# Kernel optimization log

Measured on AMD Instinct MI355X. Metric: run time of the kernel, lower is better.

Reference implementation:

```python
import jax, jax.numpy as jnp
import numpy as np

V, E, H, L = 32000, 256, 512, 2
B, S, T = 32, 128, 128

def _run_lstm(xs, layers, h0, c0):
    # xs: [B,T,in]; layers: list of (Wih[4H,in], Whh[4H,H], bih[4H], bhh[4H]); h0,c0: [L,B,H]
    def step(carry, x):
        h, c = carry
        inp = x
        hs, cs = [], []
        for l, (Wih, Whh, bih, bhh) in enumerate(layers):
            g = inp @ Wih.T + h[l] @ Whh.T + bih + bhh
            i, f, gg, o = jnp.split(g, 4, axis=-1)  # torch gate order: i, f, g, o
            cn = jax.nn.sigmoid(f) * c[l] + jax.nn.sigmoid(i) * jnp.tanh(gg)
            hn = jax.nn.sigmoid(o) * jnp.tanh(cn)
            hs.append(hn); cs.append(cn); inp = hn
        return (jnp.stack(hs), jnp.stack(cs)), inp
    (hT, cT), ys = jax.lax.scan(step, (h0, c0), jnp.swapaxes(xs, 0, 1))
    return jnp.swapaxes(ys, 0, 1), hT, cT

def setup_inputs():
    key = jax.random.key(0)
    ks = jax.random.split(key, 24)
    k = 1.0 / np.sqrt(H)
    u = lambda kk, shape: jax.random.uniform(kk, shape, jnp.float32, -k, k)
    inp = {
        "src": jax.random.randint(ks[0], (B, S), 0, V),
        "tgt": jax.random.randint(ks[1], (B, T), 0, V),
        "emb": jax.random.normal(ks[2], (V, E), jnp.float32) * 0.02,
        "Wout": u(ks[3], (V, H)),
        "bout": u(ks[4], (V,)),
    }
    i = 5
    for pre in ("enc", "dec"):
        for l in range(L):
            din = E if l == 0 else H
            inp[pre + "_Wih" + str(l)] = u(ks[i], (4 * H, din)); i += 1
            inp[pre + "_Whh" + str(l)] = u(ks[i], (4 * H, H)); i += 1
            inp[pre + "_bih" + str(l)] = u(ks[i], (4 * H,)); i += 1
            inp[pre + "_bhh" + str(l)] = u(ks[i], (4 * H,)); i += 1
    return inp

def reference(src, tgt, emb, Wout, bout,
              enc_Wih0, enc_Whh0, enc_bih0, enc_bhh0,
              enc_Wih1, enc_Whh1, enc_bih1, enc_bhh1,
              dec_Wih0, dec_Whh0, dec_bih0, dec_bhh0,
              dec_Wih1, dec_Whh1, dec_bih1, dec_bhh1):
    enc_layers = [(enc_Wih0, enc_Whh0, enc_bih0, enc_bhh0),
                  (enc_Wih1, enc_Whh1, enc_bih1, enc_bhh1)]
    dec_layers = [(dec_Wih0, dec_Whh0, dec_bih0, dec_bhh0),
                  (dec_Wih1, dec_Whh1, dec_bih1, dec_bhh1)]
    h0 = jnp.zeros((L, src.shape[0], H), jnp.float32)
    c0 = jnp.zeros_like(h0)
    src_embed = emb[src]                                   # [B,S,E]; dropout = identity (eval)
    _, hT, cT = _run_lstm(src_embed, enc_layers, h0, c0)
    tgt_embed = emb[tgt]                                   # full teacher forcing (ratio=1.0)
    dec_out, _, _ = _run_lstm(tgt_embed, dec_layers, hT, cT)  # [B,T,H]
    logits = jnp.einsum('bth,vh->btv', dec_out, Wout) + bout  # [B,T,V]
    return logits
```

## Files before the change

kernel.cpp:

```cpp
#include <hip/hip_runtime.h>
#include <math.h>

#define Bsz 32
#define Hd  512
#define SEQ 128
#define G4H 2048
#define BARSTRIDE 32
#define SLOT 16384

typedef __attribute__((ext_vector_type(8))) short bf16x8;
typedef __attribute__((ext_vector_type(4))) float f32x4;
typedef __attribute__((ext_vector_type(4))) unsigned short us4;

__device__ __forceinline__ void gload16(const void* g, void* l) {
  __builtin_amdgcn_global_load_lds(
      (const __attribute__((address_space(1))) unsigned int*)g,
      (__attribute__((address_space(3))) unsigned int*)l, 16, 0, 0);
}

__global__ __launch_bounds__(256) void bias_sum_k(const float* __restrict__ a,
                                                  const float* __restrict__ b,
                                                  float* __restrict__ out) {
  int i = blockIdx.x * 256 + threadIdx.x;
  if (i < G4H) out[i] = a[i] + b[i];
}

__global__ __launch_bounds__(256) void embed_k(const int* __restrict__ idx,
                                               const float* __restrict__ emb,
                                               float* __restrict__ out) {
  int t = blockIdx.x * 256 + threadIdx.x;
  int m = t >> 6, e4 = (t & 63) << 2;
  *(float4*)&out[(size_t)m * 256 + e4] =
      *(const float4*)&emb[(size_t)idx[m] * 256 + e4];
}

__global__ __launch_bounds__(256) void split_k(const float* __restrict__ X,
                                               unsigned short* __restrict__ hi,
                                               unsigned short* __restrict__ lo) {
  int i = (blockIdx.x * 256 + threadIdx.x) << 2;
  float4 x = *(const float4*)&X[i];
  const float* xp = (const float*)&x;
  us4 h, l;
  #pragma unroll
  for (int e = 0; e < 4; ++e) {
    float v = xp[e];
    unsigned int u = __float_as_uint(v);
    unsigned int hr = (u + 0x7fffu + ((u >> 16) & 1u)) & 0xffff0000u;
    h[e] = (unsigned short)(hr >> 16);
    float rem = v - __uint_as_float(hr);
    unsigned int u2 = __float_as_uint(rem);
    l[e] = (unsigned short)((u2 + 0x7fffu + ((u2 >> 16) & 1u)) >> 16);
  }
  *(us4*)&hi[i] = h;
  *(us4*)&lo[i] = l;
}

__global__ __launch_bounds__(256) void pack_wbf_k(const float* __restrict__ W,
                                                  unsigned short* __restrict__ out) {
  __shared__ float Wl[16][512];
  const int blk = blockIdx.x, tid = threadIdx.x;
  #pragma unroll
  for (int r = 0; r < 16; ++r) {
    int j = (r >> 2) * 512 + blk * 4 + (r & 3);
    Wl[r][tid]       = W[(size_t)j * 512 + tid];
    Wl[r][tid + 256] = W[(size_t)j * 512 + tid + 256];
  }
  __syncthreads();
  for (int idx = tid; idx < 8192; idx += 256) {
    int kf = idx >> 9, l = (idx >> 3) & 63, e = idx & 7;
    int col = l & 15;
    int kpos = (kf << 5) + ((l >> 4) << 3) + e;
    float v = Wl[col][kpos];
    unsigned int uu = __float_as_uint(v);
    unsigned int hr = (uu + 0x7fffu + ((uu >> 16) & 1u)) & 0xffff0000u;
    float rem = v - __uint_as_float(hr);
    unsigned int u2 = __float_as_uint(rem);
    out[(size_t)blk * 16384 + idx] = (unsigned short)(hr >> 16);
    out[(size_t)blk * 16384 + 8192 + idx] =
        (unsigned short)((u2 + 0x7fffu + ((u2 >> 16) & 1u)) >> 16);
  }
}

__global__ __launch_bounds__(256)
void gemm_bfs_k(const unsigned short* __restrict__ Ahi,
                const unsigned short* __restrict__ Alo,
                const unsigned short* __restrict__ Bhi,
                const unsigned short* __restrict__ Blo,
                const float* __restrict__ bias,
                float* __restrict__ C, int K, int ldc, int amode)
{
  __shared__ unsigned short Ash[4096], Asl[4096];
  __shared__ unsigned short Bsh[4096], Bsl[4096];
  const int tid = threadIdx.x;
  const int m0 = blockIdx.x << 7, n0 = blockIdx.y << 7;
  const int lane = tid & 63, wave = tid >> 6;
  const int wr = wave >> 1, wc = wave & 1;
  const int srow = wave * 32 + (lane >> 2);
  const int sk = (lane & 3) << 3;
  const int ldse = wave * 1024 + lane * 8;
  const int fr = lane & 15, fk = (lane >> 4) << 3;

  const int r1 = m0 + srow, r2 = m0 + srow + 16;
  const size_t ra1 = amode ? ((size_t)(r1 & 127) * 32 + (r1 >> 7)) * 512 : (size_t)r1 * K;
  const size_t ra2 = amode ? ((size_t)(r2 & 127) * 32 + (r2 >> 7)) * 512 : (size_t)r2 * K;
  const size_t rb1 = (size_t)(n0 + srow) * K, rb2 = (size_t)(n0 + srow + 16) * K;

  f32x4 acc[4][4];
  #pragma unroll
  for (int a = 0; a < 4; ++a)
    #pragma unroll
    for (int b = 0; b < 4; ++b) acc[a][b] = (f32x4){0.f, 0.f, 0.f, 0.f};

  #pragma unroll 1
  for (int kt = 0; kt < K; kt += 32) {
    gload16(Ahi + ra1 + kt + sk, &Ash[ldse]);
    gload16(Ahi + ra2 + kt + sk, &Ash[ldse + 512]);
    gload16(Alo + ra1 + kt + sk, &Asl[ldse]);
    gload16(Alo + ra2 + kt + sk, &Asl[ldse + 512]);
    gload16(Bhi + rb1 + kt + sk, &Bsh[ldse]);
    gload16(Bhi + rb2 + kt + sk, &Bsh[ldse + 512]);
    gload16(Blo + rb1 + kt + sk, &Bsl[ldse]);
    gload16(Blo + rb2 + kt + sk, &Bsl[ldse + 512]);
    __syncthreads();
    bf16x8 afh[4], afl[4], bfh[4], bfl[4];
    #pragma unroll
    for (int mf = 0; mf < 4; ++mf) {
      afh[mf] = *(const bf16x8*)&Ash[(wr * 64 + mf * 16 + fr) * 32 + fk];
      afl[mf] = *(const bf16x8*)&Asl[(wr * 64 + mf * 16 + fr) * 32 + fk];
    }
    #pragma unroll
    for (int nf = 0; nf < 4; ++nf) {
      bfh[nf] = *(const bf16x8*)&Bsh[(wc * 64 + nf * 16 + fr) * 32 + fk];
      bfl[nf] = *(const bf16x8*)&Bsl[(wc * 64 + nf * 16 + fr) * 32 + fk];
    }
    #pragma unroll
    for (int mf = 0; mf < 4; ++mf)
      #pragma unroll
      for (int nf = 0; nf < 4; ++nf) {
        acc[mf][nf] = __builtin_amdgcn_mfma_f32_16x16x32_bf16(afh[mf], bfh[nf],
                                                              acc[mf][nf], 0, 0, 0);
        acc[mf][nf] = __builtin_amdgcn_mfma_f32_16x16x32_bf16(afh[mf], bfl[nf],
                                                              acc[mf][nf], 0, 0, 0);
        acc[mf][nf] = __builtin_amdgcn_mfma_f32_16x16x32_bf16(afl[mf], bfh[nf],
                                                              acc[mf][nf], 0, 0, 0);
      }
    __syncthreads();
  }

  const int rgrp = (lane >> 4) << 2;
  #pragma unroll
  for (int nf = 0; nf < 4; ++nf) {
    int n = n0 + wc * 64 + nf * 16 + fr;
    float bn = bias[n];
    #pragma unroll
    for (int mf = 0; mf < 4; ++mf) {
      #pragma unroll
      for (int r = 0; r < 4; ++r) {
        int m = m0 + wr * 64 + mf * 16 + rgrp + r;
        C[(size_t)m * ldc + n] = acc[mf][nf][r] + bn;
      }
    }
  }
}

__device__ __forceinline__ void pollwait(const int* arr, int target) {
  const int tid = threadIdx.x;
  if (tid < 64) {
    const int* p0 = &arr[tid * BARSTRIDE];
    const int* p1 = &arr[(tid + 64) * BARSTRIDE];
    for (;;) {
      int a = __hip_atomic_load(p0, __ATOMIC_RELAXED, __HIP_MEMORY_SCOPE_AGENT);
      int b = __hip_atomic_load(p1, __ATOMIC_RELAXED, __HIP_MEMORY_SCOPE_AGENT);
      if (__all(min(a, b) >= target)) break;
      __builtin_amdgcn_s_sleep(1);
    }
  }
  __syncthreads();
}

__global__ __launch_bounds__(256, 1)
void lstm_seq_k(const unsigned short* __restrict__ pw0,
                const unsigned short* __restrict__ pw1a,
                const unsigned short* __restrict__ pw1b,
                const float* __restrict__ x0pre,
                const float* __restrict__ bias1,
                unsigned short* __restrict__ h0hi, unsigned short* __restrict__ h0lo,
                unsigned short* __restrict__ h1hi, unsigned short* __restrict__ h1lo,
                const unsigned short* __restrict__ h0ihi, const unsigned short* __restrict__ h0ilo,
                const unsigned short* __restrict__ h1ihi, const unsigned short* __restrict__ h1ilo,
                const float* __restrict__ c0init, const float* __restrict__ c1init,
                float* __restrict__ c0fin, float* __restrict__ c1fin,
                int* __restrict__ flagbase)
{
  __shared__ unsigned short wlds[49152];
  __shared__ float gpart[3264];
  __shared__ float gx[256];
  __shared__ unsigned short hstage[256];

  const int blk = blockIdx.x, tid = threadIdx.x;
  const int dom = blk & 1, cb = blk >> 1;
  const int bb0 = dom << 4;
  int* flag = flagbase + dom * 4096;
  const int w = tid >> 6, lane = tid & 63;
  const int fr = lane & 15, fgk = (lane >> 4) << 3;

  {
    const uint4* s0 = (const uint4*)(pw0 + (size_t)cb * 16384);
    const uint4* s1 = (const uint4*)(pw1a + (size_t)cb * 16384);
    const uint4* s2 = (const uint4*)(pw1b + (size_t)cb * 16384);
    uint4* d = (uint4*)wlds;
    for (int i = tid; i < 2048; i += 256) {
      d[i] = s0[i]; d[2048 + i] = s1[i]; d[4096 + i] = s2[i];
    }
  }

  const int b2 = tid & 15, cl = (tid >> 4) & 3;
  const int nn = cb * 4 + cl;
  const int gb = bb0 + b2;
  float creg = 0.f, bv0 = 0.f, bv1 = 0.f, bv2 = 0.f, bv3 = 0.f;
  if (tid < 64) {
    creg = c0init[gb * 512 + nn];
  } else if (tid < 128) {
    creg = c1init[gb * 512 + nn];
    bv0 = bias1[nn]; bv1 = bias1[512 + nn];
    bv2 = bias1[1024 + nn]; bv3 = bias1[1536 + nn];
  }
  const int xcol = tid & 15, xb = (tid >> 4) & 15;
  const int xj = (xcol >> 2) * 512 + cb * 4 + (xcol & 3);
  const int xgb = bb0 + xb;
  __syncthreads();

  #pragma unroll 1
  for (int u = 0; u <= SEQ; ++u) {
    const bool doL0 = (u < SEQ), doL1 = (u >= 1);

    float xv = doL0 ? x0pre[((size_t)xgb * SEQ + u) * G4H + xj] : 0.f;

    if (u > 0) pollwait(flag, u);

    if (doL0) gx[xcol * 16 + xb] = xv;

    const unsigned short* hAh = (u == 0) ? h0ihi : h0hi + (size_t)(u - 1) * SLOT;
    const unsigned short* hAl = (u == 0) ? h0ilo : h0lo + (size_t)(u - 1) * SLOT;
    const unsigned short* hBh = (u <= 1) ? h1ihi : h1hi + (size_t)(u - 2) * SLOT;
    const unsigned short* hBl = (u <= 1) ? h1ilo : h1lo + (size_t)(u - 2) * SLOT;

    f32x4 acc[3];
    acc[0] = (f32x4){0.f, 0.f, 0.f, 0.f};
    acc[1] = (f32x4){0.f, 0.f, 0.f, 0.f};
    acc[2] = (f32x4){0.f, 0.f, 0.f, 0.f};

    #pragma unroll
    for (int q = 0; q < 4; ++q) {
      const int kf = (w << 2) + q;
      const int ko = (kf << 5) + fgk;
      const int wko = (kf << 9) + lane * 8;
      const size_t arow = (size_t)(bb0 + fr) * 512 + ko;
      bf16x8 ah = *(const bf16x8*)&hAh[arow];
      bf16x8 al = *(const bf16x8*)&hAl[arow];
      if (doL0) {
        bf16x8 bh = *(const bf16x8*)&wlds[wko];
        bf16x8 bl = *(const bf16x8*)&wlds[8192 + wko];
        acc[0] = __builtin_amdgcn_mfma_f32_16x16x32_bf16(ah, bh, acc[0], 0, 0, 0);
        acc[0] = __builtin_amdgcn_mfma_f32_16x16x32_bf16(ah, bl, acc[0], 0, 0, 0);
        acc[0] = __builtin_amdgcn_mfma_f32_16x16x32_bf16(al, bh, acc[0], 0, 0, 0);
      }
      if (doL1) {
        bf16x8 bh = *(const bf16x8*)&wlds[16384 + wko];
        bf16x8 bl = *(const bf16x8*)&wlds[16384 + 8192 + wko];
        acc[1] = __builtin_amdgcn_mfma_f32_16x16x32_bf16(ah, bh, acc[1], 0, 0, 0);
        acc[1] = __builtin_amdgcn_mfma_f32_16x16x32_bf16(ah, bl, acc[1], 0, 0, 0);
        acc[1] = __builtin_amdgcn_mfma_f32_16x16x32_bf16(al, bh, acc[1], 0, 0, 0);
        bf16x8 ch = *(const bf16x8*)&hBh[arow];
        bf16x8 cl8 = *(const bf16x8*)&hBl[arow];
        bf16x8 dh = *(const bf16x8*)&wlds[32768 + wko];
        bf16x8 dl = *(const bf16x8*)&wlds[32768 + 8192 + wko];
        acc[2] = __builtin_amdgcn_mfma_f32_16x16x32_bf16(ch, dh, acc[2], 0, 0, 0);
        acc[2] = __builtin_amdgcn_mfma_f32_16x16x32_bf16(ch, dl, acc[2], 0, 0, 0);
        acc[2] = __builtin_amdgcn_mfma_f32_16x16x32_bf16(cl8, dh, acc[2], 0, 0, 0);
      }
    }

    #pragma unroll
    for (int m = 0; m < 3; ++m)
      #pragma unroll
      for (int j = 0; j < 4; ++j)
        gpart[(m * 4 + w) * 272 + ((lane >> 4) * 4 + j) * 17 + fr] = acc[m][j];
    __syncthreads();

    if (tid < 64 && doL0) {
      float g[4];
      #pragma unroll
      for (int gt = 0; gt < 4; ++gt) {
        float s = gx[(gt * 4 + cl) * 16 + b2];
        #pragma unroll
        for (int ww = 0; ww < 4; ++ww)
          s += gpart[ww * 272 + b2 * 17 + gt * 4 + cl];
        g[gt] = s;
      }
      float i_ = 1.f / (1.f + expf(-g[0]));
      float f_ = 1.f / (1.f + expf(-g[1]));
      float gg = tanhf(g[2]);
      float o_ = 1.f / (1.f + expf(-g[3]));
      float cn = f_ * creg + i_ * gg;
      float hn = o_ * tanhf(cn);
      creg = cn;
      unsigned int uu = __float_as_uint(hn);
      unsigned int hr = (uu + 0x7fffu + ((uu >> 16) & 1u)) & 0xffff0000u;
      float rem = hn - __uint_as_float(hr);
      unsigned int u2 = __float_as_uint(rem);
      hstage[(0 * 16 + b2) * 4 + cl] = (unsigned short)(hr >> 16);
      hstage[(1 * 16 + b2) * 4 + cl] =
          (unsigned short)((u2 + 0x7fffu + ((u2 >> 16) & 1u)) >> 16);
    } else if (tid >= 64 && tid < 128 && doL1) {
      float g[4];
      #pragma unroll
      for (int gt = 0; gt < 4; ++gt) {
        float s = 0.f;
        #pragma unroll
        for (int ww = 0; ww < 4; ++ww)
          s += gpart[(4 + ww) * 272 + b2 * 17 + gt * 4 + cl]
             + gpart[(8 + ww) * 272 + b2 * 17 + gt * 4 + cl];
        g[gt] = s;
      }
      g[0] += bv0; g[1] += bv1; g[2] += bv2; g[3] += bv3;
      float i_ = 1.f / (1.f + expf(-g[0]));
      float f_ = 1.f / (1.f + expf(-g[1]));
      float gg = tanhf(g[2]);
      float o_ = 1.f / (1.f + expf(-g[3]));
      float cn = f_ * creg + i_ * gg;
      float hn = o_ * tanhf(cn);
      creg = cn;
      unsigned int uu = __float_as_uint(hn);
      unsigned int hr = (uu + 0x7fffu + ((uu >> 16) & 1u)) & 0xffff0000u;
      float rem = hn - __uint_as_float(hr);
      unsigned int u2 = __float_as_uint(rem);
      hstage[(2 * 16 + b2) * 4 + cl] = (unsigned short)(hr >> 16);
      hstage[(3 * 16 + b2) * 4 + cl] =
          (unsigned short)((u2 + 0x7fffu + ((u2 >> 16) & 1u)) >> 16);
    }
    __syncthreads();

    if (tid < 64) {
      int layer = (tid >> 5) & 1, hl = (tid >> 4) & 1, bb = tid & 15;
      bool go = layer ? doL1 : doL0;
      if (go) {
        unsigned long long v =
            *(const unsigned long long*)&hstage[((layer * 2 + hl) * 16 + bb) * 4];
        unsigned short* arr = layer ? (hl ? h1lo : h1hi) : (hl ? h0lo : h0hi);
        int slot = layer ? (u - 1) : u;
        __hip_atomic_store(
            (unsigned long long*)&arr[(size_t)slot * SLOT + (bb0 + bb) * 512 + cb * 4],
            v, __ATOMIC_RELAXED, __HIP_MEMORY_SCOPE_AGENT);
      }
    }
    asm volatile("s_waitcnt vmcnt(0)" ::: "memory");
    __syncthreads();
    if (tid == 0)
      __hip_atomic_store(&flag[cb * BARSTRIDE], u + 1,
                         __ATOMIC_RELAXED, __HIP_MEMORY_SCOPE_AGENT);
  }

  if (tid < 64)        c0fin[gb * 512 + nn] = creg;
  else if (tid < 128)  c1fin[gb * 512 + nn] = creg;
}

extern "C" void kernel_launch(void* const* d_in, const int* in_sizes, int n_in,
                              void* d_out, int out_size, void* d_ws, size_t ws_size,
                              hipStream_t stream) {
  const int*   src  = (const int*)d_in[0];
  const int*   tgt  = (const int*)d_in[1];
  const float* emb  = (const float*)d_in[2];
  const float* Wout = (const float*)d_in[3];
  const float* bout = (const float*)d_in[4];
  const float* eWih0 = (const float*)d_in[5];
  const float* eWhh0 = (const float*)d_in[6];
  const float* ebih0 = (const float*)d_in[7];
  const float* ebhh0 = (const float*)d_in[8];
  const float* eWih1 = (const float*)d_in[9];
  const float* eWhh1 = (const float*)d_in[10];
  const float* ebih1 = (const float*)d_in[11];
  const float* ebhh1 = (const float*)d_in[12];
  const float* dWih0 = (const float*)d_in[13];
  const float* dWhh0 = (const float*)d_in[14];
  const float* dbih0 = (const float*)d_in[15];
  const float* dbhh0 = (const float*)d_in[16];
  const float* dWih1 = (const float*)d_in[17];
  const float* dWhh1 = (const float*)d_in[18];
  const float* dbih1 = (const float*)d_in[19];
  const float* dbhh1 = (const float*)d_in[20];

  if (ws_size < 86376448ull) return;

  float* ws = (float*)d_ws;
  char*  wsb = (char*)d_ws;
  unsigned short* PK   = (unsigned short*)(wsb + 37748736);
  unsigned short* PW0E = PK;
  unsigned short* PW1AE = PK + 2097152;
  unsigned short* PW1BE = PK + 4194304;
  unsigned short* PW0D = PK + 6291456;
  unsigned short* PW1AD = PK + 8388608;
  unsigned short* PW1BD = PK + 10485760;
  const size_t OFF_EMB  = 0;
  const size_t OFF_X0   = 1048576;
  const size_t OFF_BS0E = 15728640;
  const size_t OFF_B1E  = 15730688;
  const size_t OFF_BS0D = 15732736;
  const size_t OFF_B1D  = 15734784;
  const size_t OFF_Z    = 15736832;
  unsigned short* Ehi  = (unsigned short*)(wsb + 63176704);
  unsigned short* Elo  = (unsigned short*)(wsb + 65273856);
  unsigned short* WIhi = (unsigned short*)(wsb + 67371008);
  unsigned short* WIlo = (unsigned short*)(wsb + 68419584);
  unsigned short* H0hi = (unsigned short*)(wsb + 69468160);
  unsigned short* H0lo = (unsigned short*)(wsb + 73662464);
  unsigned short* H1hi = (unsigned short*)(wsb + 77856768);
  unsigned short* H1lo = (unsigned short*)(wsb + 82051072);
  unsigned short* Bhi  = (unsigned short*)(wsb + 0);
  unsigned short* Blo  = (unsigned short*)(wsb + 32768000);
  float* C0f = (float*)(wsb + 86245376);
  float* C1f = (float*)(wsb + 86310912);
  const unsigned short* ZU = (const unsigned short*)(ws + OFF_Z);
  const float* ZF = ws + OFF_Z;

  int* fb = (int*)(wsb + 63012864);
  int* eF = fb;
  int* dF = fb + 8192;

  pack_wbf_k<<<128, 256, 0, stream>>>(eWhh0, PW0E);
  pack_wbf_k<<<128, 256, 0, stream>>>(eWih1, PW1AE);
  pack_wbf_k<<<128, 256, 0, stream>>>(eWhh1, PW1BE);
  pack_wbf_k<<<128, 256, 0, stream>>>(dWhh0, PW0D);
  pack_wbf_k<<<128, 256, 0, stream>>>(dWih1, PW1AD);
  pack_wbf_k<<<128, 256, 0, stream>>>(dWhh1, PW1BD);
  bias_sum_k<<<8, 256, 0, stream>>>(ebih0, ebhh0, ws + OFF_BS0E);
  bias_sum_k<<<8, 256, 0, stream>>>(ebih1, ebhh1, ws + OFF_B1E);
  bias_sum_k<<<8, 256, 0, stream>>>(dbih0, dbhh0, ws + OFF_BS0D);
  bias_sum_k<<<8, 256, 0, stream>>>(dbih1, dbhh1, ws + OFF_B1D);

  hipMemsetAsync(ws + OFF_Z, 0, 131072, stream);

  embed_k<<<1024, 256, 0, stream>>>(src, emb, ws + OFF_EMB);
  split_k<<<1024, 256, 0, stream>>>(ws + OFF_EMB, Ehi, Elo);
  split_k<<<512, 256, 0, stream>>>(eWih0, WIhi, WIlo);
  gemm_bfs_k<<<dim3(32, 16), 256, 0, stream>>>(Ehi, Elo, WIhi, WIlo,
                                               ws + OFF_BS0E, ws + OFF_X0, 256, 2048, 0);
  lstm_seq_k<<<256, 256, 0, stream>>>(PW0E, PW1AE, PW1BE,
                                      ws + OFF_X0, ws + OFF_B1E,
                                      H0hi, H0lo, H1hi, H1lo,
                                      ZU, ZU, ZU, ZU,
                                      ZF, ZF,
                                      C0f, C1f,
                                      eF);

  embed_k<<<1024, 256, 0, stream>>>(tgt, emb, ws + OFF_EMB);
  split_k<<<1024, 256, 0, stream>>>(ws + OFF_EMB, Ehi, Elo);
  split_k<<<512, 256, 0, stream>>>(dWih0, WIhi, WIlo);
  gemm_bfs_k<<<dim3(32, 16), 256, 0, stream>>>(Ehi, Elo, WIhi, WIlo,
                                               ws + OFF_BS0D, ws + OFF_X0, 256, 2048, 0);
  lstm_seq_k<<<256, 256, 0, stream>>>(PW0D, PW1AD, PW1BD,
                                      ws + OFF_X0, ws + OFF_B1D,
                                      H0hi, H0lo, H1hi, H1lo,
                                      H0hi + (size_t)127 * SLOT, H0lo + (size_t)127 * SLOT,
                                      H1hi + (size_t)127 * SLOT, H1lo + (size_t)127 * SLOT,
                                      C0f, C1f,
                                      C0f, C1f,
                                      dF);

  split_k<<<16000, 256, 0, stream>>>(Wout, Bhi, Blo);
  gemm_bfs_k<<<dim3(32, 250), 256, 0, stream>>>(H1hi, H1lo, Bhi, Blo,
                                                bout, (float*)d_out, 512, 32000, 1);
}
```

Baseline: 1.913 ms.

## Enlarge GEMM tiles to 256x256 and fuse small setup kernels

The split-bf16 GEMM grows from 128x128 tiles with 256 threads to 256x256 tiles with 512 threads. Each wave now computes a 128x64 sub-tile, so every loaded operand is reused more and the vocabulary projection needs fewer blocks. The separate weight-pack, bias-sum, embedding-gather and split launches are merged into a few multi-target kernels, and both encoder and decoder input weights are split up front. The cost is 64KB of LDS and more accumulator registers per block, which lowers occupancy and leaves fewer blocks for the small input GEMMs.

```diff
diff --git a/kernel.cpp b/kernel.cpp
--- a/kernel.cpp
+++ b/kernel.cpp
@@ -18,20 +18,39 @@
       (__attribute__((address_space(3))) unsigned int*)l, 16, 0, 0);
 }
 
-__global__ __launch_bounds__(256) void bias_sum_k(const float* __restrict__ a,
-                                                  const float* __restrict__ b,
-                                                  float* __restrict__ out) {
+__global__ __launch_bounds__(256) void bias_all_k(const float* a0, const float* b0, float* o0,
+                                                  const float* a1, const float* b1, float* o1,
+                                                  const float* a2, const float* b2, float* o2,
+                                                  const float* a3, const float* b3, float* o3) {
   int i = blockIdx.x * 256 + threadIdx.x;
-  if (i < G4H) out[i] = a[i] + b[i];
-}
-
-__global__ __launch_bounds__(256) void embed_k(const int* __restrict__ idx,
-                                               const float* __restrict__ emb,
-                                               float* __restrict__ out) {
+  int sel = i >> 11, j = i & 2047;
+  const float* a = sel == 0 ? a0 : sel == 1 ? a1 : sel == 2 ? a2 : a3;
+  const float* b = sel == 0 ? b0 : sel == 1 ? b1 : sel == 2 ? b2 : b3;
+  float* o       = sel == 0 ? o0 : sel == 1 ? o1 : sel == 2 ? o2 : o3;
+  o[j] = a[j] + b[j];
+}
+
+__global__ __launch_bounds__(256) void embed_split_k(const int* __restrict__ idx,
+                                                     const float* __restrict__ emb,
+                                                     unsigned short* __restrict__ hi,
+                                                     unsigned short* __restrict__ lo) {
   int t = blockIdx.x * 256 + threadIdx.x;
   int m = t >> 6, e4 = (t & 63) << 2;
-  *(float4*)&out[(size_t)m * 256 + e4] =
-      *(const float4*)&emb[(size_t)idx[m] * 256 + e4];
+  float4 x = *(const float4*)&emb[(size_t)idx[m] * 256 + e4];
+  const float* xp = (const float*)&x;
+  us4 h, l;
+  #pragma unroll
+  for (int e = 0; e < 4; ++e) {
+    float v = xp[e];
+    unsigned int u = __float_as_uint(v);
+    unsigned int hr = (u + 0x7fffu + ((u >> 16) & 1u)) & 0xffff0000u;
+    h[e] = (unsigned short)(hr >> 16);
+    float rem = v - __uint_as_float(hr);
+    unsigned int u2 = __float_as_uint(rem);
+    l[e] = (unsigned short)((u2 + 0x7fffu + ((u2 >> 16) & 1u)) >> 16);
+  }
+  *(us4*)&hi[(size_t)m * 256 + e4] = h;
+  *(us4*)&lo[(size_t)m * 256 + e4] = l;
 }
 
 __global__ __launch_bounds__(256) void split_k(const float* __restrict__ X,
@@ -55,10 +74,42 @@
   *(us4*)&lo[i] = l;
 }
 
-__global__ __launch_bounds__(256) void pack_wbf_k(const float* __restrict__ W,
-                                                  unsigned short* __restrict__ out) {
+__global__ __launch_bounds__(256) void wsplit2_k(const float* __restrict__ X0,
+                                                 unsigned short* __restrict__ h0, unsigned short* __restrict__ l0,
+                                                 const float* __restrict__ X1,
+                                                 unsigned short* __restrict__ h1, unsigned short* __restrict__ l1) {
+  int bi = blockIdx.x;
+  const float* X = bi < 512 ? X0 : X1;
+  unsigned short* hh = bi < 512 ? h0 : h1;
+  unsigned short* ll = bi < 512 ? l0 : l1;
+  int i = (((bi & 511) * 256) + threadIdx.x) << 2;
+  float4 x = *(const float4*)&X[i];
+  const float* xp = (const float*)&x;
+  us4 h, l;
+  #pragma unroll
+  for (int e = 0; e < 4; ++e) {
+    float v = xp[e];
+    unsigned int u = __float_as_uint(v);
+    unsigned int hr = (u + 0x7fffu + ((u >> 16) & 1u)) & 0xffff0000u;
+    h[e] = (unsigned short)(hr >> 16);
+    float rem = v - __uint_as_float(hr);
+    unsigned int u2 = __float_as_uint(rem);
+    l[e] = (unsigned short)((u2 + 0x7fffu + ((u2 >> 16) & 1u)) >> 16);
+  }
+  *(us4*)&hh[i] = h;
+  *(us4*)&ll[i] = l;
+}
+
+__global__ __launch_bounds__(256) void pack_all_k(const float* w0, unsigned short* o0,
+                                                  const float* w1, unsigned short* o1,
+                                                  const float* w2, unsigned short* o2,
+                                                  const float* w3, unsigned short* o3,
+                                                  const float* w4, unsigned short* o4,
+                                                  const float* w5, unsigned short* o5) {
   __shared__ float Wl[16][512];
-  const int blk = blockIdx.x, tid = threadIdx.x;
+  const int sel = blockIdx.x >> 7, blk = blockIdx.x & 127, tid = threadIdx.x;
+  const float* W = sel == 0 ? w0 : sel == 1 ? w1 : sel == 2 ? w2 : sel == 3 ? w3 : sel == 4 ? w4 : w5;
+  unsigned short* out = sel == 0 ? o0 : sel == 1 ? o1 : sel == 2 ? o2 : sel == 3 ? o3 : sel == 4 ? o4 : o5;
   #pragma unroll
   for (int r = 0; r < 16; ++r) {
     int j = (r >> 2) * 512 + blk * 4 + (r & 3);
@@ -81,20 +132,20 @@
   }
 }
 
-__global__ __launch_bounds__(256)
-void gemm_bfs_k(const unsigned short* __restrict__ Ahi,
-                const unsigned short* __restrict__ Alo,
-                const unsigned short* __restrict__ Bhi,
-                const unsigned short* __restrict__ Blo,
-                const float* __restrict__ bias,
-                float* __restrict__ C, int K, int ldc, int amode)
+__global__ __launch_bounds__(512)
+void gemm_bfs2_k(const unsigned short* __restrict__ Ahi,
+                 const unsigned short* __restrict__ Alo,
+                 const unsigned short* __restrict__ Bhi,
+                 const unsigned short* __restrict__ Blo,
+                 const float* __restrict__ bias,
+                 float* __restrict__ C, int K, int ldc, int amode)
 {
-  __shared__ unsigned short Ash[4096], Asl[4096];
-  __shared__ unsigned short Bsh[4096], Bsl[4096];
+  __shared__ unsigned short Ash[8192], Asl[8192];
+  __shared__ unsigned short Bsh[8192], Bsl[8192];
   const int tid = threadIdx.x;
-  const int m0 = blockIdx.x << 7, n0 = blockIdx.y << 7;
+  const int m0 = blockIdx.x << 8, n0 = blockIdx.y << 8;
   const int lane = tid & 63, wave = tid >> 6;
-  const int wr = wave >> 1, wc = wave & 1;
+  const int wm = wave >> 2, wn = wave & 3;
   const int srow = wave * 32 + (lane >> 2);
   const int sk = (lane & 3) << 3;
   const int ldse = wave * 1024 + lane * 8;
@@ -105,9 +156,9 @@
   const size_t ra2 = amode ? ((size_t)(r2 & 127) * 32 + (r2 >> 7)) * 512 : (size_t)r2 * K;
   const size_t rb1 = (size_t)(n0 + srow) * K, rb2 = (size_t)(n0 + srow + 16) * K;
 
-  f32x4 acc[4][4];
+  f32x4 acc[8][4];
   #pragma unroll
-  for (int a = 0; a < 4; ++a)
+  for (int a = 0; a < 8; ++a)
     #pragma unroll
     for (int b = 0; b < 4; ++b) acc[a][b] = (f32x4){0.f, 0.f, 0.f, 0.f};
 
@@ -122,41 +173,39 @@
     gload16(Blo + rb1 + kt + sk, &Bsl[ldse]);
     gload16(Blo + rb2 + kt + sk, &Bsl[ldse + 512]);
     __syncthreads();
-    bf16x8 afh[4], afl[4], bfh[4], bfl[4];
-    #pragma unroll
-    for (int mf = 0; mf < 4; ++mf) {
-      afh[mf] = *(const bf16x8*)&Ash[(wr * 64 + mf * 16 + fr) * 32 + fk];
-      afl[mf] = *(const bf16x8*)&Asl[(wr * 64 + mf * 16 + fr) * 32 + fk];
-    }
+    bf16x8 bfh[4], bfl[4];
     #pragma unroll
     for (int nf = 0; nf < 4; ++nf) {
-      bfh[nf] = *(const bf16x8*)&Bsh[(wc * 64 + nf * 16 + fr) * 32 + fk];
-      bfl[nf] = *(const bf16x8*)&Bsl[(wc * 64 + nf * 16 + fr) * 32 + fk];
+      bfh[nf] = *(const bf16x8*)&Bsh[(wn * 64 + nf * 16 + fr) * 32 + fk];
+      bfl[nf] = *(const bf16x8*)&Bsl[(wn * 64 + nf * 16 + fr) * 32 + fk];
     }
     #pragma unroll
-    for (int mf = 0; mf < 4; ++mf)
+    for (int mf = 0; mf < 8; ++mf) {
+      bf16x8 afh = *(const bf16x8*)&Ash[(wm * 128 + mf * 16 + fr) * 32 + fk];
+      bf16x8 afl = *(const bf16x8*)&Asl[(wm * 128 + mf * 16 + fr) * 32 + fk];
       #pragma unroll
       for (int nf = 0; nf < 4; ++nf) {
-        acc[mf][nf] = __builtin_amdgcn_mfma_f32_16x16x32_bf16(afh[mf], bfh[nf],
+        acc[mf][nf] = __builtin_amdgcn_mfma_f32_16x16x32_bf16(afh, bfh[nf],
                                                               acc[mf][nf], 0, 0, 0);
-        acc[mf][nf] = __builtin_amdgcn_mfma_f32_16x16x32_bf16(afh[mf], bfl[nf],
+        acc[mf][nf] = __builtin_amdgcn_mfma_f32_16x16x32_bf16(afh, bfl[nf],
                                                               acc[mf][nf], 0, 0, 0);
-        acc[mf][nf] = __builtin_amdgcn_mfma_f32_16x16x32_bf16(afl[mf], bfh[nf],
+        acc[mf][nf] = __builtin_amdgcn_mfma_f32_16x16x32_bf16(afl, bfh[nf],
                                                               acc[mf][nf], 0, 0, 0);
       }
+    }
     __syncthreads();
   }
 
   const int rgrp = (lane >> 4) << 2;
   #pragma unroll
   for (int nf = 0; nf < 4; ++nf) {
-    int n = n0 + wc * 64 + nf * 16 + fr;
+    int n = n0 + wn * 64 + nf * 16 + fr;
     float bn = bias[n];
     #pragma unroll
-    for (int mf = 0; mf < 4; ++mf) {
+    for (int mf = 0; mf < 8; ++mf) {
       #pragma unroll
       for (int r = 0; r < 4; ++r) {
-        int m = m0 + wr * 64 + mf * 16 + rgrp + r;
+        int m = m0 + wm * 128 + mf * 16 + rgrp + r;
         C[(size_t)m * ldc + n] = acc[mf][nf][r] + bn;
       }
     }
@@ -401,7 +450,6 @@
   unsigned short* PW0D = PK + 6291456;
   unsigned short* PW1AD = PK + 8388608;
   unsigned short* PW1BD = PK + 10485760;
-  const size_t OFF_EMB  = 0;
   const size_t OFF_X0   = 1048576;
   const size_t OFF_BS0E = 15728640;
   const size_t OFF_B1E  = 15730688;
@@ -410,8 +458,10 @@
   const size_t OFF_Z    = 15736832;
   unsigned short* Ehi  = (unsigned short*)(wsb + 63176704);
   unsigned short* Elo  = (unsigned short*)(wsb + 65273856);
-  unsigned short* WIhi = (unsigned short*)(wsb + 67371008);
-  unsigned short* WIlo = (unsigned short*)(wsb + 68419584);
+  unsigned short* WIhiE = (unsigned short*)(wsb + 67371008);
+  unsigned short* WIloE = (unsigned short*)(wsb + 68419584);
+  unsigned short* WIhiD = (unsigned short*)(wsb + 0);
+  unsigned short* WIloD = (unsigned short*)(wsb + 1048576);
   unsigned short* H0hi = (unsigned short*)(wsb + 69468160);
   unsigned short* H0lo = (unsigned short*)(wsb + 73662464);
   unsigned short* H1hi = (unsigned short*)(wsb + 77856768);
@@ -427,23 +477,18 @@
   int* eF = fb;
   int* dF = fb + 8192;
 
-  pack_wbf_k<<<128, 256, 0, stream>>>(eWhh0, PW0E);
-  pack_wbf_k<<<128, 256, 0, stream>>>(eWih1, PW1AE);
-  pack_wbf_k<<<128, 256, 0, stream>>>(eWhh1, PW1BE);
-  pack_wbf_k<<<128, 256, 0, stream>>>(dWhh0, PW0D);
-  pack_wbf_k<<<128, 256, 0, stream>>>(dWih1, PW1AD);
-  pack_wbf_k<<<128, 256, 0, stream>>>(dWhh1, PW1BD);
-  bias_sum_k<<<8, 256, 0, stream>>>(ebih0, ebhh0, ws + OFF_BS0E);
-  bias_sum_k<<<8, 256, 0, stream>>>(ebih1, ebhh1, ws + OFF_B1E);
-  bias_sum_k<<<8, 256, 0, stream>>>(dbih0, dbhh0, ws + OFF_BS0D);
-  bias_sum_k<<<8, 256, 0, stream>>>(dbih1, dbhh1, ws + OFF_B1D);
+  pack_all_k<<<768, 256, 0, stream>>>(eWhh0, PW0E, eWih1, PW1AE, eWhh1, PW1BE,
+                                      dWhh0, PW0D, dWih1, PW1AD, dWhh1, PW1BD);
+  bias_all_k<<<32, 256, 0, stream>>>(ebih0, ebhh0, ws + OFF_BS0E,
+                                     ebih1, ebhh1, ws + OFF_B1E,
+                                     dbih0, dbhh0, ws + OFF_BS0D,
+                                     dbih1, dbhh1, ws + OFF_B1D);
+  wsplit2_k<<<1024, 256, 0, stream>>>(eWih0, WIhiE, WIloE, dWih0, WIhiD, WIloD);
 
   hipMemsetAsync(ws + OFF_Z, 0, 131072, stream);
 
-  embed_k<<<1024, 256, 0, stream>>>(src, emb, ws + OFF_EMB);
-  split_k<<<1024, 256, 0, stream>>>(ws + OFF_EMB, Ehi, Elo);
-  split_k<<<512, 256, 0, stream>>>(eWih0, WIhi, WIlo);
-  gemm_bfs_k<<<dim3(32, 16), 256, 0, stream>>>(Ehi, Elo, WIhi, WIlo,
+  embed_split_k<<<1024, 256, 0, stream>>>(src, emb, Ehi, Elo);
+  gemm_bfs2_k<<<dim3(16, 8), 512, 0, stream>>>(Ehi, Elo, WIhiE, WIloE,
                                                ws + OFF_BS0E, ws + OFF_X0, 256, 2048, 0);
   lstm_seq_k<<<256, 256, 0, stream>>>(PW0E, PW1AE, PW1BE,
                                       ws + OFF_X0, ws + OFF_B1E,
@@ -453,10 +498,8 @@
                                       C0f, C1f,
                                       eF);
 
-  embed_k<<<1024, 256, 0, stream>>>(tgt, emb, ws + OFF_EMB);
-  split_k<<<1024, 256, 0, stream>>>(ws + OFF_EMB, Ehi, Elo);
-  split_k<<<512, 256, 0, stream>>>(dWih0, WIhi, WIlo);
-  gemm_bfs_k<<<dim3(32, 16), 256, 0, stream>>>(Ehi, Elo, WIhi, WIlo,
+  embed_split_k<<<1024, 256, 0, stream>>>(tgt, emb, Ehi, Elo);
+  gemm_bfs2_k<<<dim3(16, 8), 512, 0, stream>>>(Ehi, Elo, WIhiD, WIloD,
                                                ws + OFF_BS0D, ws + OFF_X0, 256, 2048, 0);
   lstm_seq_k<<<256, 256, 0, stream>>>(PW0D, PW1AD, PW1BD,
                                       ws + OFF_X0, ws + OFF_B1D,
@@ -468,6 +511,6 @@
                                       dF);
 
   split_k<<<16000, 256, 0, stream>>>(Wout, Bhi, Blo);
-  gemm_bfs_k<<<dim3(32, 250), 256, 0, stream>>>(H1hi, H1lo, Bhi, Blo,
-                                                bout, (float*)d_out, 512, 32000, 1);
-}
+  gemm_bfs2_k<<<dim3(16, 125), 512, 0, stream>>>(H1hi, H1lo, Bhi, Blo,
+                                                 bout, (float*)d_out, 512, 32000, 1);
+}
```

Result: no change. 1.947 ms (+1.8%).
